# Kernel tuning notes

Hardware: AMD Instinct MI355X
Metric: run time of the kernel (lower is better)

The kernel has to match this reference:

```python
import jax, jax.numpy as jnp
import numpy as np

D = 768


def _rope(x):
    # interleaved RoPE over the FULL hidden dim (applied before head split, as in source)
    S, d = x.shape[-2], x.shape[-1]
    pos = jnp.arange(S, dtype=x.dtype)[:, None]                      # [S,1]
    theta = jnp.power(jnp.asarray(10000.0, x.dtype),
                      -2.0 * jnp.arange(d // 2, dtype=x.dtype) / d)  # [d/2]
    ang = pos * theta                                                # [S,d/2]
    cos2 = jnp.repeat(jnp.cos(ang), 2, axis=-1)                      # [S,d]
    sin2 = jnp.repeat(jnp.sin(ang), 2, axis=-1)
    x2 = jnp.stack([-x[..., 1::2], x[..., ::2]], axis=-1).reshape(x.shape)
    return x * cos2 + x2 * sin2


def _attn(q_in, kv_in, wq, bq, wk, bk, wv, bv, n_heads):
    # shared core of SelfAttention (n_heads=1) and MultiheadAttention (n_heads=8)
    B, Sq, Dm = q_in.shape
    Sk = kv_in.shape[1]
    Q = _rope(q_in @ wq + bq)
    K = _rope(kv_in @ wk + bk)
    V = kv_in @ wv + bv
    hd = Dm // n_heads
    Q = Q.reshape(B, Sq, n_heads, hd).transpose(0, 2, 1, 3)
    K = K.reshape(B, Sk, n_heads, hd).transpose(0, 2, 1, 3)
    V = V.reshape(B, Sk, n_heads, hd).transpose(0, 2, 1, 3)
    scores = jnp.einsum('bhqd,bhkd->bhqk', Q, K) * 8.0  # source multiplies by 8, no 1/sqrt(d)
    p = jax.nn.softmax(scores, axis=-1)
    out = jnp.einsum('bhqk,bhkd->bhqd', p, V)
    return out.transpose(0, 2, 1, 3).reshape(B, Sq, Dm)


def _ffn(x, w1, b1, w2, b2):
    return jax.nn.silu(x @ w1 + b1) @ w2 + b2


def _gate(x):
    # F = F * softmax(F, -1) + F
    return x * jax.nn.softmax(x, axis=-1) + x


def setup_inputs() -> dict:
    key = jax.random.key(0)
    ks = jax.random.split(key, 32)
    B, S, L = 32, 512, 100
    s = 1.0 / np.sqrt(D)

    def lin(k):
        kw, kb = jax.random.split(k)
        return (jax.random.normal(kw, (D, D), jnp.float32) * s,
                jax.random.normal(kb, (D,), jnp.float32) * 0.01)

    inp = {}
    inp['text_embedding'] = jax.random.normal(ks[0], (B, S, D), jnp.float32)
    inp['visual_ids'] = jax.random.randint(ks[1], (B, S), 0, L)
    inp['acoustic_ids'] = jax.random.randint(ks[2], (B, S), 0, L)
    # embedding tables (label_size+1 rows, last row is padding_idx -> zeros)
    vt = jax.random.normal(ks[3], (L + 1, D), jnp.float32)
    at = jax.random.normal(ks[4], (L + 1, D), jnp.float32)
    inp['vis_table'] = vt.at[L].set(0.0)
    inp['ac_table'] = at.at[L].set(0.0)
    (inp['hv_wq'], inp['hv_bq']) = lin(ks[5])
    (inp['hv_wk'], inp['hv_bk']) = lin(ks[6])
    (inp['hv_wv'], inp['hv_bv']) = lin(ks[7])
    (inp['ha_wq'], inp['ha_bq']) = lin(ks[8])
    (inp['ha_wk'], inp['ha_bk']) = lin(ks[9])
    (inp['ha_wv'], inp['ha_bv']) = lin(ks[10])
    (inp['ht_wq'], inp['ht_bq']) = lin(ks[11])
    (inp['ht_wk'], inp['ht_bk']) = lin(ks[12])
    (inp['ht_wv'], inp['ht_bv']) = lin(ks[13])
    (inp['ht_fcw'], inp['ht_fcb']) = lin(ks[14])
    (inp['ffn_w1'], inp['ffn_b1']) = lin(ks[15])
    (inp['ffn_w2'], inp['ffn_b2']) = lin(ks[16])
    kw, kb = jax.random.split(ks[17])
    inp['cat_w'] = jax.random.normal(kw, (2 * D, D), jnp.float32) * (1.0 / np.sqrt(2 * D))
    inp['cat_b'] = jax.random.normal(kb, (D,), jnp.float32) * 0.01
    return inp


def reference(text_embedding, vis_table, ac_table,
              hv_wq, hv_bq, hv_wk, hv_bk, hv_wv, hv_bv,
              ha_wq, ha_bq, ha_wk, ha_bk, ha_wv, ha_bv,
              ht_wq, ht_bq, ht_wk, ht_bk, ht_wv, ht_bv, ht_fcw, ht_fcb,
              ffn_w1, ffn_b1, ffn_w2, ffn_b2, cat_w, cat_b,
              visual_ids, acoustic_ids):
    hv = lambda q, kv: _attn(q, kv, hv_wq, hv_bq, hv_wk, hv_bk, hv_wv, hv_bv, 1)
    ha = lambda q, kv: _attn(q, kv, ha_wq, ha_bq, ha_wk, ha_bk, ha_wv, ha_bv, 1)

    visual_ = vis_table[visual_ids]       # [B,S,D]
    acoustic_ = ac_table[acoustic_ids]

    visual_ = hv(text_embedding, visual_)
    acoustic_ = ha(text_embedding, acoustic_)

    F1 = jnp.concatenate([visual_, acoustic_], axis=-1) @ cat_w + cat_b
    F1 = _ffn(_gate(F1), ffn_w1, ffn_b1, ffn_w2, ffn_b2)

    v = hv(visual_, acoustic_)
    a = ha(acoustic_, visual_)
    F2 = jnp.concatenate([v, a], axis=-1) @ cat_w + cat_b
    F2 = _ffn(_gate(F2), ffn_w1, ffn_b1, ffn_w2, ffn_b2)

    F3 = _attn(F1, text_embedding, ht_wq, ht_bq, ht_wk, ht_bk, ht_wv, ht_bv, 8)
    F3 = F3 @ ht_fcw + ht_fcb
    F3 = _ffn(_gate(F3), ffn_w1, ffn_b1, ffn_w2, ffn_b2)

    es = text_embedding + F1 + F2 + F3
    return _gate(es)
```

## Files before the change

### kernel.cpp

```cpp
#include <hip/hip_runtime.h>
#include <stdint.h>
#include <math.h>


typedef unsigned short USH;
typedef __attribute__((ext_vector_type(8))) short short8;
typedef __attribute__((ext_vector_type(4))) float floatx4;

#define MFMA16(a, b, c) __builtin_amdgcn_mfma_f32_16x16x32_bf16((a), (b), (c), 0, 0, 0)

static constexpr int NB = 32;
static constexpr int SS = 512;
static constexpr int DD = 768;
static constexpr int MM = NB * SS;

__device__ __forceinline__ float bf2f(USH h) {
    return __uint_as_float(((unsigned)h) << 16);
}
__device__ __forceinline__ USH f2bf(float x) {
    unsigned u = __float_as_uint(x);
    return (USH)((u + 0x7fffu + ((u >> 16) & 1u)) >> 16);
}
__device__ __forceinline__ void split3(float x, USH &h, USH &m, USH &l) {
    h = f2bf(x);
    const float r1 = x - bf2f(h);
    m = f2bf(r1);
    const float r2 = r1 - bf2f(m);
    l = f2bf(r2);
}
__device__ __forceinline__ void split3x8(const float* v, short8 &H, short8 &M, short8 &L) {
#pragma unroll
    for (int j = 0; j < 8; ++j) {
        USH h, m, l;
        split3(v[j], h, m, l);
        H[j] = (short)h; M[j] = (short)m; L[j] = (short)l;
    }
}
__device__ __forceinline__ uint2 pk4(USH a, USH b, USH c, USH d) {
    uint2 r;
    r.x = (unsigned)a | ((unsigned)b << 16);
    r.y = (unsigned)c | ((unsigned)d << 16);
    return r;
}

struct TransArgs {
    const float* in[13];
    USH* o0[13]; USH* o1[13]; USH* o2[13];
    int R[13];
};

__global__ __launch_bounds__(256) void trans_k(TransArgs a) {
    const int mi = blockIdx.z;
    const float* __restrict__ in = a.in[mi];
    USH* __restrict__ o0 = a.o0[mi];
    USH* __restrict__ o1 = a.o1[mi];
    USH* __restrict__ o2 = a.o2[mi];
    const int R = a.R[mi];
    const int bx = blockIdx.x, by = blockIdx.y;
    if (bx * 32 >= R) return;
    __shared__ float t[32][33];
    const int tx = threadIdx.x & 31, ty = threadIdx.x >> 5;
#pragma unroll
    for (int i = 0; i < 4; ++i)
        t[ty + i * 8][tx] = in[(size_t)(bx * 32 + ty + i * 8) * 768 + by * 32 + tx];
    __syncthreads();
#pragma unroll
    for (int i = 0; i < 4; ++i) {
        USH h, m, l;
        split3(t[tx][ty + i * 8], h, m, l);
        const size_t o = (size_t)(by * 32 + ty + i * 8) * R + bx * 32 + tx;
        o0[o] = h; o1[o] = m; o2[o] = l;
    }
}

__global__ __launch_bounds__(256) void gather_k(const int* __restrict__ ids,
                                                const float* __restrict__ table,
                                                float* __restrict__ dst) {
    const int g  = blockIdx.x * 256 + threadIdx.x;
    const int m  = g / 192;
    const int c4 = (g - m * 192) * 4;
    const int id = ids[m];
    *(float4*)(dst + (size_t)m * DD + c4) =
        *(const float4*)(table + (size_t)id * DD + c4);
}

__global__ __launch_bounds__(256) void gemm_k(
    const float* __restrict__ A0, const float* __restrict__ A1,
    const USH* __restrict__ B0, const USH* __restrict__ B1, const USH* __restrict__ B2,
    int ldb, const float* __restrict__ bias,
    float* __restrict__ C, USH* __restrict__ S0p, USH* __restrict__ S1p,
    USH* __restrict__ S2p, int K, int act, int tout, int Mc)
{
    __shared__ __align__(16) USH sA0[4096], sA1[4096], sA2[4096];
    __shared__ __align__(16) USH sB0[4096], sB1[4096], sB2[4096];

    const int tid  = threadIdx.x;
    const int lane = tid & 63;
    const int w    = tid >> 6;
    const int quad = lane >> 4, l15 = lane & 15;
    const int wm = (w >> 1) * 64, wn = (w & 1) * 64;
    const int gm0 = blockIdx.x * 128, gn0 = blockIdx.y * 128;

    const int i0 = tid * 2, i1 = tid * 2 + 1;
    const int r0 = i0 >> 2, c0 = (i0 & 3) << 3;
    const int r1 = i1 >> 2, c1 = (i1 & 3) << 3;

    const floatx4 zero = {0.f, 0.f, 0.f, 0.f};
    floatx4 acc[4][4];
#pragma unroll
    for (int i = 0; i < 4; ++i)
#pragma unroll
        for (int j = 0; j < 4; ++j) acc[i][j] = zero;

    for (int k0 = 0; k0 < K; k0 += 32) {
        const float* __restrict__ A = (k0 < 768) ? A0 : A1;
        const int kof = (k0 < 768) ? k0 : (k0 - 768);

        *(uint4*)&sB0[r0 * 32 + c0] = *(const uint4*)(B0 + (size_t)(gn0 + r0) * ldb + k0 + c0);
        *(uint4*)&sB0[r1 * 32 + c1] = *(const uint4*)(B0 + (size_t)(gn0 + r1) * ldb + k0 + c1);
        *(uint4*)&sB1[r0 * 32 + c0] = *(const uint4*)(B1 + (size_t)(gn0 + r0) * ldb + k0 + c0);
        *(uint4*)&sB1[r1 * 32 + c1] = *(const uint4*)(B1 + (size_t)(gn0 + r1) * ldb + k0 + c1);
        *(uint4*)&sB2[r0 * 32 + c0] = *(const uint4*)(B2 + (size_t)(gn0 + r0) * ldb + k0 + c0);
        *(uint4*)&sB2[r1 * 32 + c1] = *(const uint4*)(B2 + (size_t)(gn0 + r1) * ldb + k0 + c1);

#pragma unroll
        for (int u = 0; u < 4; ++u) {
            const int idx = tid + u * 256;
            const int r = idx >> 3, c = (idx & 7) * 4;
            const float4 v = *(const float4*)(A + (size_t)(gm0 + r) * 768 + kof + c);
            USH h[4], m[4], l[4];
            split3(v.x, h[0], m[0], l[0]);
            split3(v.y, h[1], m[1], l[1]);
            split3(v.z, h[2], m[2], l[2]);
            split3(v.w, h[3], m[3], l[3]);
            *(uint2*)&sA0[r * 32 + c] = pk4(h[0], h[1], h[2], h[3]);
            *(uint2*)&sA1[r * 32 + c] = pk4(m[0], m[1], m[2], m[3]);
            *(uint2*)&sA2[r * 32 + c] = pk4(l[0], l[1], l[2], l[3]);
        }
        __syncthreads();

        short8 a0[4], a1f[4], a2[4], b0[4], b1f[4], b2[4];
#pragma unroll
        for (int t = 0; t < 4; ++t) {
            const int ao = (wm + t * 16 + l15) * 32 + quad * 8;
            const int bo = (wn + t * 16 + l15) * 32 + quad * 8;
            a0[t]  = *(const short8*)&sA0[ao];
            a1f[t] = *(const short8*)&sA1[ao];
            a2[t]  = *(const short8*)&sA2[ao];
            b0[t]  = *(const short8*)&sB0[bo];
            b1f[t] = *(const short8*)&sB1[bo];
            b2[t]  = *(const short8*)&sB2[bo];
        }
#pragma unroll
        for (int i = 0; i < 4; ++i)
#pragma unroll
            for (int j = 0; j < 4; ++j) acc[i][j] = MFMA16(a0[i],  b0[j],  acc[i][j]);
#pragma unroll
        for (int i = 0; i < 4; ++i)
#pragma unroll
            for (int j = 0; j < 4; ++j) acc[i][j] = MFMA16(a0[i],  b1f[j], acc[i][j]);
#pragma unroll
        for (int i = 0; i < 4; ++i)
#pragma unroll
            for (int j = 0; j < 4; ++j) acc[i][j] = MFMA16(a1f[i], b0[j],  acc[i][j]);
#pragma unroll
        for (int i = 0; i < 4; ++i)
#pragma unroll
            for (int j = 0; j < 4; ++j) acc[i][j] = MFMA16(a0[i],  b2[j],  acc[i][j]);
#pragma unroll
        for (int i = 0; i < 4; ++i)
#pragma unroll
            for (int j = 0; j < 4; ++j) acc[i][j] = MFMA16(a2[i],  b0[j],  acc[i][j]);
#pragma unroll
        for (int i = 0; i < 4; ++i)
#pragma unroll
            for (int j = 0; j < 4; ++j) acc[i][j] = MFMA16(a1f[i], b1f[j], acc[i][j]);
        __syncthreads();
    }

#pragma unroll
    for (int j = 0; j < 4; ++j) {
        const int col = gn0 + wn + j * 16 + l15;
        const float bv = bias[col];
#pragma unroll
        for (int i = 0; i < 4; ++i) {
#pragma unroll
            for (int r = 0; r < 4; ++r) {
                const int row = gm0 + wm + i * 16 + quad * 4 + r;
                float x = acc[i][j][r] + bv;
                if (act == 1) {
                    const float s = 1.0f / (1.0f + expf(-x));
                    x = x * s;
                }
                if (tout == 1) {
                    USH hh, mm2, ll;
                    split3(x, hh, mm2, ll);
                    const size_t o = (size_t)col * Mc + row;
                    S0p[o] = hh; S1p[o] = mm2; S2p[o] = ll;
                } else if (tout == 2) {
                    C[(size_t)col * Mc + row] = x;
                } else {
                    C[(size_t)row * 768 + col] = x;
                }
            }
        }
    }
}

__global__ __launch_bounds__(256) void tab_k(float* __restrict__ tab) {
    const int p = blockIdx.x * 256 + threadIdx.x;
    const int s = p / 384;
    const int i = p - s * 384;
    const float ef = (-2.0f * (float)i) / 768.0f;
    const float th = (float)pow(10000.0, (double)ef);
    const float ang = (float)s * th;
    float sn, cs;
    sincosf(ang, &sn, &cs);
    tab[2 * p]     = cs;
    tab[2 * p + 1] = sn;
}

__global__ __launch_bounds__(256) void rope_k(float* __restrict__ X) {
    const int p = blockIdx.x * 256 + threadIdx.x;
    const int m = p / 384;
    const int i = p - m * 384;
    const int s = m & (SS - 1);
    const float ef = (-2.0f * (float)i) / 768.0f;
    const float th = (float)pow(10000.0, (double)ef);
    const float ang = (float)s * th;
    float sn, cs;
    sincosf(ang, &sn, &cs);
    float2 x = *(float2*)(X + (size_t)m * DD + 2 * i);
    float2 y;
    y.x = x.x * cs - x.y * sn;
    y.y = x.y * cs + x.x * sn;
    *(float2*)(X + (size_t)m * DD + 2 * i) = y;
}

__global__ __launch_bounds__(256) void rope_tab_k(float* __restrict__ X,
                                                  const float* __restrict__ tab) {
    const int p = blockIdx.x * 256 + threadIdx.x;
    const int m = p / 384;
    const int i = p - m * 384;
    const int s = m & (SS - 1);
    const float2 t = *(const float2*)(tab + 2 * (s * 384 + i));
    float2 x = *(float2*)(X + (size_t)m * DD + 2 * i);
    float2 y;
    y.x = x.x * t.x - x.y * t.y;
    y.y = x.y * t.x + x.x * t.y;
    *(float2*)(X + (size_t)m * DD + 2 * i) = y;
}

__global__ __launch_bounds__(256) void rope_split_tab_k(
    const float* __restrict__ X, const float* __restrict__ tab,
    USH* __restrict__ P0, USH* __restrict__ P1, USH* __restrict__ P2)
{
    const int p = blockIdx.x * 256 + threadIdx.x;
    const int m = p / 384;
    const int i = p - m * 384;
    const int s = m & (SS - 1);
    const float2 t = *(const float2*)(tab + 2 * (s * 384 + i));
    const float2 x = *(const float2*)(X + (size_t)m * DD + 2 * i);
    float2 y;
    y.x = x.x * t.x - x.y * t.y;
    y.y = x.y * t.x + x.x * t.y;
    USH h0, m0, l0, h1, m1, l1;
    split3(y.x, h0, m0, l0);
    split3(y.y, h1, m1, l1);
    const size_t o = (size_t)m * DD + 2 * i;
    *(unsigned*)&P0[o] = (unsigned)h0 | ((unsigned)h1 << 16);
    *(unsigned*)&P1[o] = (unsigned)m0 | ((unsigned)m1 << 16);
    *(unsigned*)&P2[o] = (unsigned)l0 | ((unsigned)l1 << 16);
}

__global__ __launch_bounds__(256) void attn_fast_k(
    const float* __restrict__ Q,
    const USH* __restrict__ KH, const USH* __restrict__ KM, const USH* __restrict__ KL,
    const USH* __restrict__ VH, const USH* __restrict__ VM, const USH* __restrict__ VL,
    float* __restrict__ O, int H, int hd, int Mc)
{
    __shared__ __align__(16) float S[16][520];
    __shared__ __align__(16) USH P2buf[16 * 520];
    __shared__ float red[16][16];
    __shared__ float stat[16];

    const int tid  = threadIdx.x;
    const int lane = tid & 63;
    const int w    = tid >> 6;
    const int quad = lane >> 4, l15 = lane & 15;
    const int b = blockIdx.y / H;
    const int h = blockIdx.y - b * H;
    const int q0 = blockIdx.x * 16;

    const floatx4 zero = {0.f, 0.f, 0.f, 0.f};

    floatx4 acc[8];
#pragma unroll
    for (int t = 0; t < 8; ++t) acc[t] = zero;

    const size_t qbase  = ((size_t)(b * SS + q0 + l15)) * DD + h * hd;
    const size_t kstrip = ((size_t)(b * SS + w * 128 + l15)) * DD + h * hd;
    const int nks = hd >> 5;
    for (int ks = 0; ks < nks; ++ks) {
        const int co = ks * 32 + quad * 8;
        float qv[8];
        *(float4*)&qv[0] = *(const float4*)(Q + qbase + co);
        *(float4*)&qv[4] = *(const float4*)(Q + qbase + co + 4);
        short8 qh, qm, ql;
        split3x8(qv, qh, qm, ql);

        size_t ka = kstrip + co;
        short8 khc = *(const short8*)&KH[ka];
        short8 kmc = *(const short8*)&KM[ka];
        short8 klc = *(const short8*)&KL[ka];
#pragma unroll
        for (int t = 0; t < 8; ++t) {
            short8 khn = khc, kmn = kmc, kln = klc;
            if (t < 7) {
                const size_t kb = ka + (size_t)(t + 1) * 16 * DD;
                khn = *(const short8*)&KH[kb];
                kmn = *(const short8*)&KM[kb];
                kln = *(const short8*)&KL[kb];
            }
            acc[t] = MFMA16(qh, khc, acc[t]);
            acc[t] = MFMA16(qh, kmc, acc[t]);
            acc[t] = MFMA16(qm, khc, acc[t]);
            acc[t] = MFMA16(qh, klc, acc[t]);
            acc[t] = MFMA16(ql, khc, acc[t]);
            acc[t] = MFMA16(qm, kmc, acc[t]);
            __builtin_amdgcn_sched_barrier(0);
            khc = khn; kmc = kmn; klc = kln;
        }
    }
#pragma unroll
    for (int t = 0; t < 8; ++t)
#pragma unroll
        for (int r = 0; r < 4; ++r)
            S[quad * 4 + r][w * 128 + t * 16 + l15] = acc[t][r] * 8.0f;
    __syncthreads();

    const int row = tid >> 4, c16 = tid & 15;
    const int cb = c16 * 32;
    float mx = -3.4e38f;
#pragma unroll 8
    for (int c = 0; c < 32; ++c) mx = fmaxf(mx, S[row][cb + c]);
    red[row][c16] = mx;
    __syncthreads();
    if (c16 == 0) {
        float m2 = red[row][0];
#pragma unroll
        for (int j = 1; j < 16; ++j) m2 = fmaxf(m2, red[row][j]);
        stat[row] = m2;
    }
    __syncthreads();
    mx = stat[row];
    float ev[32];
    float sum = 0.f;
#pragma unroll 8
    for (int c = 0; c < 32; ++c) {
        ev[c] = expf(S[row][cb + c] - mx);
        sum += ev[c];
    }
    red[row][c16] = sum;
    __syncthreads();
    if (c16 == 0) {
        float s2 = 0.f;
#pragma unroll
        for (int j = 0; j < 16; ++j) s2 += red[row][j];
        stat[row] = s2;
    }
    __syncthreads();
    const float den = stat[row];
    USH* const P0 = (USH*)&S[0][0];
    USH* const P1 = P0 + 16 * 520;
    USH* const P2 = P2buf;
#pragma unroll 8
    for (int c = 0; c < 32; ++c) {
        const float pr = ev[c] / den;
        USH hh, mm, ll;
        split3(pr, hh, mm, ll);
        P0[row * 520 + cb + c] = hh;
        P1[row * 520 + cb + c] = mm;
        P2[row * 520 + cb + c] = ll;
    }
    __syncthreads();

    const int nnt = hd >> 4;
    for (int nt = w; nt < nnt; nt += 4) {
        floatx4 o = zero;
        const int colg = h * hd + nt * 16 + l15;
        const size_t vb = (size_t)colg * Mc + b * SS;
#pragma unroll 2
        for (int ks = 0; ks < 16; ++ks) {
            const int ko = ks * 32 + quad * 8;
            const short8 ph = *(const short8*)&P0[l15 * 520 + ko];
            const short8 pm = *(const short8*)&P1[l15 * 520 + ko];
            const short8 pl = *(const short8*)&P2[l15 * 520 + ko];
            const short8 vh = *(const short8*)&VH[vb + ko];
            const short8 vm = *(const short8*)&VM[vb + ko];
            const short8 vl = *(const short8*)&VL[vb + ko];
            o = MFMA16(ph, vh, o);
            o = MFMA16(ph, vm, o);
            o = MFMA16(pm, vh, o);
            o = MFMA16(ph, vl, o);
            o = MFMA16(pl, vh, o);
            o = MFMA16(pm, vm, o);
        }
#pragma unroll
        for (int r = 0; r < 4; ++r) {
            const int orow = b * SS + q0 + quad * 4 + r;
            O[(size_t)orow * 768 + colg] = o[r];
        }
    }
}

__global__ __launch_bounds__(256) void attn_k(
    const float* __restrict__ Q, const float* __restrict__ Kp,
    const float* __restrict__ Vt, float* __restrict__ O,
    int H, int hd, int Mc)
{
    __shared__ __align__(16) float S[16][520];
    __shared__ __align__(16) USH P2buf[16 * 520];
    __shared__ float red[16][16];
    __shared__ float stat[16];

    const int tid  = threadIdx.x;
    const int lane = tid & 63;
    const int w    = tid >> 6;
    const int quad = lane >> 4, l15 = lane & 15;
    const int b = blockIdx.y / H;
    const int h = blockIdx.y - b * H;
    const int q0 = blockIdx.x * 16;

    const floatx4 zero = {0.f, 0.f, 0.f, 0.f};

    floatx4 acc[8];
#pragma unroll
    for (int t = 0; t < 8; ++t) acc[t] = zero;

    const size_t qbase = ((size_t)(b * SS + q0 + l15)) * DD + h * hd;
    const int nks = hd >> 5;
    for (int ks = 0; ks < nks; ++ks) {
        const int co = ks * 32 + quad * 8;
        float qv[8];
        *(float4*)&qv[0] = *(const float4*)(Q + qbase + co);
        *(float4*)&qv[4] = *(const float4*)(Q + qbase + co + 4);
        short8 qh, qm, ql;
        split3x8(qv, qh, qm, ql);
#pragma unroll
        for (int t = 0; t < 8; ++t) {
            const size_t kb = ((size_t)(b * SS + w * 128 + t * 16 + l15)) * DD + h * hd + co;
            float kv[8];
            *(float4*)&kv[0] = *(const float4*)(Kp + kb);
            *(float4*)&kv[4] = *(const float4*)(Kp + kb + 4);
            short8 kh, km, kl;
            split3x8(kv, kh, km, kl);
            acc[t] = MFMA16(qh, kh, acc[t]);
            acc[t] = MFMA16(qh, km, acc[t]);
            acc[t] = MFMA16(qm, kh, acc[t]);
            acc[t] = MFMA16(qh, kl, acc[t]);
            acc[t] = MFMA16(ql, kh, acc[t]);
            acc[t] = MFMA16(qm, km, acc[t]);
        }
    }
#pragma unroll
    for (int t = 0; t < 8; ++t)
#pragma unroll
        for (int r = 0; r < 4; ++r)
            S[quad * 4 + r][w * 128 + t * 16 + l15] = acc[t][r] * 8.0f;
    __syncthreads();

    const int row = tid >> 4, c16 = tid & 15;
    const int cb = c16 * 32;
    float mx = -3.4e38f;
#pragma unroll 8
    for (int c = 0; c < 32; ++c) mx = fmaxf(mx, S[row][cb + c]);
    red[row][c16] = mx;
    __syncthreads();
    if (c16 == 0) {
        float m2 = red[row][0];
#pragma unroll
        for (int j = 1; j < 16; ++j) m2 = fmaxf(m2, red[row][j]);
        stat[row] = m2;
    }
    __syncthreads();
    mx = stat[row];
    float ev[32];
    float sum = 0.f;
#pragma unroll 8
    for (int c = 0; c < 32; ++c) {
        ev[c] = expf(S[row][cb + c] - mx);
        sum += ev[c];
    }
    red[row][c16] = sum;
    __syncthreads();
    if (c16 == 0) {
        float s2 = 0.f;
#pragma unroll
        for (int j = 0; j < 16; ++j) s2 += red[row][j];
        stat[row] = s2;
    }
    __syncthreads();
    const float den = stat[row];
    USH* const P0 = (USH*)&S[0][0];
    USH* const P1 = P0 + 16 * 520;
    USH* const P2 = P2buf;
#pragma unroll 8
    for (int c = 0; c < 32; ++c) {
        const float pr = ev[c] / den;
        USH hh, mm, ll;
        split3(pr, hh, mm, ll);
        P0[row * 520 + cb + c] = hh;
        P1[row * 520 + cb + c] = mm;
        P2[row * 520 + cb + c] = ll;
    }
    __syncthreads();

    const int nnt = hd >> 4;
    for (int nt = w; nt < nnt; nt += 4) {
        floatx4 o = zero;
        const int colg = h * hd + nt * 16 + l15;
        const size_t vb = (size_t)colg * Mc + b * SS;
        for (int ks = 0; ks < 16; ++ks) {
            const int ko = ks * 32 + quad * 8;
            const short8 ph = *(const short8*)&P0[l15 * 520 + ko];
            const short8 pm = *(const short8*)&P1[l15 * 520 + ko];
            const short8 pl = *(const short8*)&P2[l15 * 520 + ko];
            float vv[8];
            *(float4*)&vv[0] = *(const float4*)(Vt + vb + ko);
            *(float4*)&vv[4] = *(const float4*)(Vt + vb + ko + 4);
            short8 vh, vm, vl;
            split3x8(vv, vh, vm, vl);
            o = MFMA16(ph, vh, o);
            o = MFMA16(ph, vm, o);
            o = MFMA16(pm, vh, o);
            o = MFMA16(ph, vl, o);
            o = MFMA16(pl, vh, o);
            o = MFMA16(pm, vm, o);
        }
#pragma unroll
        for (int r = 0; r < 4; ++r) {
            const int orow = b * SS + q0 + quad * 4 + r;
            O[(size_t)orow * 768 + colg] = o[r];
        }
    }
}

__global__ __launch_bounds__(256) void gate_k(float* __restrict__ X) {
    __shared__ float red[256];
    const int r = blockIdx.x, tid = threadIdx.x;
    const size_t base = (size_t)r * DD;
    float x[3];
#pragma unroll
    for (int j = 0; j < 3; ++j) x[j] = X[base + tid + j * 256];
    float mx = fmaxf(x[0], fmaxf(x[1], x[2]));
    red[tid] = mx;
    __syncthreads();
    for (int s = 128; s > 0; s >>= 1) {
        if (tid < s) red[tid] = fmaxf(red[tid], red[tid + s]);
        __syncthreads();
    }
    mx = red[0];
    __syncthreads();
    float e[3];
    float sum = 0.f;
#pragma unroll
    for (int j = 0; j < 3; ++j) { e[j] = expf(x[j] - mx); sum += e[j]; }
    red[tid] = sum;
    __syncthreads();
    for (int s = 128; s > 0; s >>= 1) {
        if (tid < s) red[tid] += red[tid + s];
        __syncthreads();
    }
    const float den = red[0];
#pragma unroll
    for (int j = 0; j < 3; ++j)
        X[base + tid + j * 256] = x[j] * (e[j] / den) + x[j];
}

__global__ __launch_bounds__(256) void final_k(
    const float* __restrict__ text,
    const float* __restrict__ F1, const float* __restrict__ F2,
    const float* __restrict__ F3, float* __restrict__ out)
{
    __shared__ float red[256];
    const int r = blockIdx.x, tid = threadIdx.x;
    const size_t base = (size_t)r * DD;
    float x[3];
#pragma unroll
    for (int j = 0; j < 3; ++j) {
        const int c = tid + j * 256;
        x[j] = ((text[base + c] + F1[base + c]) + F2[base + c]) + F3[base + c];
    }
    float mx = fmaxf(x[0], fmaxf(x[1], x[2]));
    red[tid] = mx;
    __syncthreads();
    for (int s = 128; s > 0; s >>= 1) {
        if (tid < s) red[tid] = fmaxf(red[tid], red[tid + s]);
        __syncthreads();
    }
    mx = red[0];
    __syncthreads();
    float e[3];
    float sum = 0.f;
#pragma unroll
    for (int j = 0; j < 3; ++j) { e[j] = expf(x[j] - mx); sum += e[j]; }
    red[tid] = sum;
    __syncthreads();
    for (int s = 128; s > 0; s >>= 1) {
        if (tid < s) red[tid] += red[tid + s];
        __syncthreads();
    }
    const float den = red[0];
#pragma unroll
    for (int j = 0; j < 3; ++j) {
        const int c = tid + j * 256;
        out[base + c] = x[j] * (e[j] / den) + x[j];
    }
}

extern "C" void kernel_launch(void* const* d_in, const int* in_sizes, int n_in,
                              void* d_out, int out_size, void* d_ws, size_t ws_size,
                              hipStream_t stream)
{
    (void)in_sizes; (void)n_in; (void)out_size;

    const float* text    = (const float*)d_in[0];
    const int*   vis_ids = (const int*)d_in[1];
    const int*   ac_ids  = (const int*)d_in[2];
    const float* vis_tab = (const float*)d_in[3];
    const float* ac_tab  = (const float*)d_in[4];
    const float* hv_wq = (const float*)d_in[5],  *hv_bq = (const float*)d_in[6];
    const float* hv_wk = (const float*)d_in[7],  *hv_bk = (const float*)d_in[8];
    const float* hv_wv = (const float*)d_in[9],  *hv_bv = (const float*)d_in[10];
    const float* ha_wq = (const float*)d_in[11], *ha_bq = (const float*)d_in[12];
    const float* ha_wk = (const float*)d_in[13], *ha_bk = (const float*)d_in[14];
    const float* ha_wv = (const float*)d_in[15], *ha_bv = (const float*)d_in[16];
    const float* ht_wq = (const float*)d_in[17], *ht_bq = (const float*)d_in[18];
    const float* ht_wk = (const float*)d_in[19], *ht_bk = (const float*)d_in[20];
    const float* ht_wv = (const float*)d_in[21], *ht_bv = (const float*)d_in[22];
    const float* ht_fcw = (const float*)d_in[23], *ht_fcb = (const float*)d_in[24];
    const float* ffn_w1 = (const float*)d_in[25], *ffn_b1 = (const float*)d_in[26];
    const float* ffn_w2 = (const float*)d_in[27], *ffn_b2 = (const float*)d_in[28];
    const float* cat_w  = (const float*)d_in[29], *cat_b  = (const float*)d_in[30];

    const size_t SQ   = (size_t)768 * 768;
    const size_t WUSH = 3 * (12 * SQ + (size_t)768 * 1536);
    const size_t TABF = (size_t)512 * 384 * 2;
    int Mc = 0, fast = 0;
    for (int cand = MM; cand >= 512; cand >>= 1) {
        const size_t nf = WUSH * sizeof(USH) + TABF * 4 + (size_t)cand * 768 * 28;
        const size_t ns = WUSH * sizeof(USH) + (size_t)cand * 768 * 24;
        if (nf <= ws_size) { Mc = cand; fast = 1; break; }
        if (ns <= ws_size) { Mc = cand; fast = 0; break; }
    }
    if (Mc == 0) return;
    const int nchunk = MM / Mc;
    const int chB    = Mc / SS;

    USH* p = (USH*)d_ws;
    USH *wt0[13], *wt1[13], *wt2[13];
    for (int i = 0; i < 13; ++i) {
        const size_t sz = (i == 12) ? (size_t)768 * 1536 : SQ;
        wt0[i] = p; p += sz;
        wt1[i] = p; p += sz;
        wt2[i] = p; p += sz;
    }

    TransArgs ta;
    const float* tin[13] = {hv_wq, hv_wk, hv_wv, ha_wq, ha_wk, ha_wv,
                            ht_wq, ht_wk, ht_wv, ht_fcw, ffn_w1, ffn_w2, cat_w};
    for (int i = 0; i < 13; ++i) {
        ta.in[i] = tin[i]; ta.o0[i] = wt0[i]; ta.o1[i] = wt1[i]; ta.o2[i] = wt2[i];
        ta.R[i] = (i == 12) ? 1536 : 768;
    }
    trans_k<<<dim3(48, 24, 13), 256, 0, stream>>>(ta);

    const size_t PSZ = (size_t)Mc * 768;
    const dim3 gg(Mc / 128, DD / 128), gb(256);
    const int ropeg = Mc * 384 / 256;
    const float* NULF = nullptr;
    USH* const NUSH = nullptr;

    if (fast) {
        float* tab = (float*)p;
        float* fp  = tab + TABF;
        float *A_ = fp + 0 * PSZ, *B_ = fp + 1 * PSZ;
        float *C_ = fp + 2 * PSZ, *F_ = fp + 3 * PSZ;
        USH* KH = (USH*)(fp + 4 * PSZ);
        USH* KM = KH + PSZ;  USH* KL = KM + PSZ;
        USH* VH = KL + PSZ;  USH* VM = VH + PSZ;  USH* VL = VM + PSZ;

        tab_k<<<(512 * 384) / 256, 256, 0, stream>>>(tab);

#define GEMM(A0P, A1P, WI, LDB, BIAS, CP, KK, ACT) \
    gemm_k<<<gg, gb, 0, stream>>>(A0P, A1P, wt0[WI], wt1[WI], wt2[WI], LDB, BIAS, \
                                  CP, NUSH, NUSH, NUSH, KK, ACT, 0, Mc)
#define GEMMV(A0P, WI, BIAS) \
    gemm_k<<<gg, gb, 0, stream>>>(A0P, NULF, wt0[WI], wt1[WI], wt2[WI], 768, BIAS, \
                                  (float*)nullptr, VH, VM, VL, 768, 0, 1, Mc)
#define ROPE(XP)  rope_tab_k<<<ropeg, 256, 0, stream>>>(XP, tab)
#define RSPL(XP)  rope_split_tab_k<<<ropeg, 256, 0, stream>>>(XP, tab, KH, KM, KL)
#define ATTNF(QP, OP, HH, HD) \
    attn_fast_k<<<dim3(SS / 16, chB * (HH)), 256, 0, stream>>>(QP, KH, KM, KL, \
                                                  VH, VM, VL, OP, HH, HD, Mc)
#define GATE(XP) gate_k<<<Mc, 256, 0, stream>>>(XP)

        for (int c = 0; c < nchunk; ++c) {
            const float* tx = text + (size_t)c * PSZ;
            const int* vi = vis_ids + (size_t)c * Mc;
            const int* ai = ac_ids  + (size_t)c * Mc;
            float* outc = (float*)d_out + (size_t)c * PSZ;

            gather_k<<<Mc * 192 / 256, 256, 0, stream>>>(vi, vis_tab, A_);
            gather_k<<<Mc * 192 / 256, 256, 0, stream>>>(ai, ac_tab, B_);

            GEMM(tx, NULF, 0, 768, hv_bq, C_, 768, 0);
            GEMM(A_, NULF, 1, 768, hv_bk, outc, 768, 0);
            GEMMV(A_, 2, hv_bv);
            ROPE(C_); RSPL(outc);
            ATTNF(C_, F_, 1, 768);

            GEMM(tx, NULF, 3, 768, ha_bq, C_, 768, 0);
            GEMM(B_, NULF, 4, 768, ha_bk, outc, 768, 0);
            GEMMV(B_, 5, ha_bv);
            ROPE(C_); RSPL(outc);
            ATTNF(C_, A_, 1, 768);

            GEMM(F_, NULF, 0, 768, hv_bq, C_, 768, 0);
            GEMM(A_, NULF, 1, 768, hv_bk, outc, 768, 0);
            GEMMV(A_, 2, hv_bv);
            ROPE(C_); RSPL(outc);
            ATTNF(C_, C_, 1, 768);

            GEMM(A_, NULF, 3, 768, ha_bq, B_, 768, 0);
            GEMM(F_, NULF, 4, 768, ha_bk, outc, 768, 0);
            GEMMV(F_, 5, ha_bv);
            ROPE(B_); RSPL(outc);
            ATTNF(B_, B_, 1, 768);

            GEMM(F_, A_, 12, 1536, cat_b, outc, 1536, 0);
            GATE(outc);
            GEMM(outc, NULF, 10, 768, ffn_b1, F_, 768, 1);
            GEMM(F_, NULF, 11, 768, ffn_b2, A_, 768, 0);

            GEMM(C_, B_, 12, 1536, cat_b, outc, 1536, 0);
            GATE(outc);
            GEMM(outc, NULF, 10, 768, ffn_b1, F_, 768, 1);
            GEMM(F_, NULF, 11, 768, ffn_b2, C_, 768, 0);

            GEMM(A_, NULF, 6, 768, ht_bq, B_, 768, 0);
            GEMM(tx, NULF, 7, 768, ht_bk, outc, 768, 0);
            GEMMV(tx, 8, ht_bv);
            ROPE(B_); RSPL(outc);
            ATTNF(B_, B_, 8, 96);
            GEMM(B_, NULF, 9, 768, ht_fcb, F_, 768, 0);
            GATE(F_);
            GEMM(F_, NULF, 10, 768, ffn_b1, B_, 768, 1);
            GEMM(B_, NULF, 11, 768, ffn_b2, F_, 768, 0);

            final_k<<<Mc, 256, 0, stream>>>(tx, A_, C_, F_, outc);
        }
#undef GEMM
#undef GEMMV
#undef ROPE
#undef RSPL
#undef ATTNF
#undef GATE
    } else {
        float* fp = (float*)p;
        float *A_ = fp + 0 * PSZ, *B_ = fp + 1 * PSZ, *C_ = fp + 2 * PSZ;
        float *D_ = fp + 3 * PSZ, *E_ = fp + 4 * PSZ, *F_ = fp + 5 * PSZ;

#define GEMM(A0P, A1P, WI, LDB, BIAS, CP, KK, ACT, TOUT) \
    gemm_k<<<gg, gb, 0, stream>>>(A0P, A1P, wt0[WI], wt1[WI], wt2[WI], LDB, BIAS, \
                                  CP, NUSH, NUSH, NUSH, KK, ACT, TOUT, Mc)
#define ROPE(XP) rope_k<<<ropeg, 256, 0, stream>>>(XP)
#define ATTN(QP, KP, VP, OP, HH, HD) \
    attn_k<<<dim3(SS / 16, chB * (HH)), 256, 0, stream>>>(QP, KP, VP, OP, HH, HD, Mc)
#define GATE(XP) gate_k<<<Mc, 256, 0, stream>>>(XP)

        for (int c = 0; c < nchunk; ++c) {
            const float* tx = text + (size_t)c * PSZ;
            const int* vi = vis_ids + (size_t)c * Mc;
            const int* ai = ac_ids  + (size_t)c * Mc;
            float* outc = (float*)d_out + (size_t)c * PSZ;

            gather_k<<<Mc * 192 / 256, 256, 0, stream>>>(vi, vis_tab, A_);
            gather_k<<<Mc * 192 / 256, 256, 0, stream>>>(ai, ac_tab, B_);

            GEMM(tx, NULF, 0, 768, hv_bq, C_, 768, 0, 0);
            GEMM(A_, NULF, 1, 768, hv_bk, D_, 768, 0, 0);
            GEMM(A_, NULF, 2, 768, hv_bv, E_, 768, 0, 2);
            ROPE(C_); ROPE(D_);
            ATTN(C_, D_, E_, F_, 1, 768);

            GEMM(tx, NULF, 3, 768, ha_bq, C_, 768, 0, 0);
            GEMM(B_, NULF, 4, 768, ha_bk, D_, 768, 0, 0);
            GEMM(B_, NULF, 5, 768, ha_bv, E_, 768, 0, 2);
            ROPE(C_); ROPE(D_);
            ATTN(C_, D_, E_, A_, 1, 768);

            GEMM(F_, NULF, 0, 768, hv_bq, C_, 768, 0, 0);
            GEMM(A_, NULF, 1, 768, hv_bk, D_, 768, 0, 0);
            GEMM(A_, NULF, 2, 768, hv_bv, E_, 768, 0, 2);
            ROPE(C_); ROPE(D_);
            ATTN(C_, D_, E_, C_, 1, 768);

            GEMM(A_, NULF, 3, 768, ha_bq, B_, 768, 0, 0);
            GEMM(F_, NULF, 4, 768, ha_bk, D_, 768, 0, 0);
            GEMM(F_, NULF, 5, 768, ha_bv, E_, 768, 0, 2);
            ROPE(B_); ROPE(D_);
            ATTN(B_, D_, E_, B_, 1, 768);

            GEMM(F_, A_, 12, 1536, cat_b, D_, 1536, 0, 0);
            GATE(D_);
            GEMM(D_, NULF, 10, 768, ffn_b1, E_, 768, 1, 0);
            GEMM(E_, NULF, 11, 768, ffn_b2, F_, 768, 0, 0);

            GEMM(C_, B_, 12, 1536, cat_b, A_, 1536, 0, 0);
            GATE(A_);
            GEMM(A_, NULF, 10, 768, ffn_b1, C_, 768, 1, 0);
            GEMM(C_, NULF, 11, 768, ffn_b2, B_, 768, 0, 0);

            GEMM(F_, NULF, 6, 768, ht_bq, C_, 768, 0, 0);
            GEMM(tx, NULF, 7, 768, ht_bk, D_, 768, 0, 0);
            GEMM(tx, NULF, 8, 768, ht_bv, E_, 768, 0, 2);
            ROPE(C_); ROPE(D_);
            ATTN(C_, D_, E_, C_, 8, 96);
            GEMM(C_, NULF, 9, 768, ht_fcb, A_, 768, 0, 0);
            GATE(A_);
            GEMM(A_, NULF, 10, 768, ffn_b1, C_, 768, 1, 0);
            GEMM(C_, NULF, 11, 768, ffn_b2, D_, 768, 0, 0);

            final_k<<<Mc, 256, 0, stream>>>(tx, F_, B_, D_, outc);
        }
#undef GEMM
#undef ROPE
#undef ATTN
#undef GATE
    }
}
```

Baseline: 7.340 ms.

## Fuse RoPE and split into GEMM epilogue, stage transposed stores, swizzle block order

Applies RoPE inside the GEMM epilogue, using a lane shuffle for the paired element and a precomputed table. This removes the separate rope_tab and rope_split kernels and their extra global round trips for Q and K. K is written directly as three bf16 split planes. The transposed V split output is staged through shared memory so global stores are coalesced, and both the GEMM and attention kernels remap block IDs across groups of eight, likely to improve cache locality. The risks are more epilogue work, such as the shuffle and table loads, and extra synchronisation in the transposed path.

```diff
diff --git a/kernel.cpp b/kernel.cpp
--- a/kernel.cpp
+++ b/kernel.cpp
@@ -82,129 +82,6 @@
     const int id = ids[m];
     *(float4*)(dst + (size_t)m * DD + c4) =
         *(const float4*)(table + (size_t)id * DD + c4);
-}
-
-__global__ __launch_bounds__(256) void gemm_k(
-    const float* __restrict__ A0, const float* __restrict__ A1,
-    const USH* __restrict__ B0, const USH* __restrict__ B1, const USH* __restrict__ B2,
-    int ldb, const float* __restrict__ bias,
-    float* __restrict__ C, USH* __restrict__ S0p, USH* __restrict__ S1p,
-    USH* __restrict__ S2p, int K, int act, int tout, int Mc)
-{
-    __shared__ __align__(16) USH sA0[4096], sA1[4096], sA2[4096];
-    __shared__ __align__(16) USH sB0[4096], sB1[4096], sB2[4096];
-
-    const int tid  = threadIdx.x;
-    const int lane = tid & 63;
-    const int w    = tid >> 6;
-    const int quad = lane >> 4, l15 = lane & 15;
-    const int wm = (w >> 1) * 64, wn = (w & 1) * 64;
-    const int gm0 = blockIdx.x * 128, gn0 = blockIdx.y * 128;
-
-    const int i0 = tid * 2, i1 = tid * 2 + 1;
-    const int r0 = i0 >> 2, c0 = (i0 & 3) << 3;
-    const int r1 = i1 >> 2, c1 = (i1 & 3) << 3;
-
-    const floatx4 zero = {0.f, 0.f, 0.f, 0.f};
-    floatx4 acc[4][4];
-#pragma unroll
-    for (int i = 0; i < 4; ++i)
-#pragma unroll
-        for (int j = 0; j < 4; ++j) acc[i][j] = zero;
-
-    for (int k0 = 0; k0 < K; k0 += 32) {
-        const float* __restrict__ A = (k0 < 768) ? A0 : A1;
-        const int kof = (k0 < 768) ? k0 : (k0 - 768);
-
-        *(uint4*)&sB0[r0 * 32 + c0] = *(const uint4*)(B0 + (size_t)(gn0 + r0) * ldb + k0 + c0);
-        *(uint4*)&sB0[r1 * 32 + c1] = *(const uint4*)(B0 + (size_t)(gn0 + r1) * ldb + k0 + c1);
-        *(uint4*)&sB1[r0 * 32 + c0] = *(const uint4*)(B1 + (size_t)(gn0 + r0) * ldb + k0 + c0);
-        *(uint4*)&sB1[r1 * 32 + c1] = *(const uint4*)(B1 + (size_t)(gn0 + r1) * ldb + k0 + c1);
-        *(uint4*)&sB2[r0 * 32 + c0] = *(const uint4*)(B2 + (size_t)(gn0 + r0) * ldb + k0 + c0);
-        *(uint4*)&sB2[r1 * 32 + c1] = *(const uint4*)(B2 + (size_t)(gn0 + r1) * ldb + k0 + c1);
-
-#pragma unroll
-        for (int u = 0; u < 4; ++u) {
-            const int idx = tid + u * 256;
-            const int r = idx >> 3, c = (idx & 7) * 4;
-            const float4 v = *(const float4*)(A + (size_t)(gm0 + r) * 768 + kof + c);
-            USH h[4], m[4], l[4];
-            split3(v.x, h[0], m[0], l[0]);
-            split3(v.y, h[1], m[1], l[1]);
-            split3(v.z, h[2], m[2], l[2]);
-            split3(v.w, h[3], m[3], l[3]);
-            *(uint2*)&sA0[r * 32 + c] = pk4(h[0], h[1], h[2], h[3]);
-            *(uint2*)&sA1[r * 32 + c] = pk4(m[0], m[1], m[2], m[3]);
-            *(uint2*)&sA2[r * 32 + c] = pk4(l[0], l[1], l[2], l[3]);
-        }
-        __syncthreads();
-
-        short8 a0[4], a1f[4], a2[4], b0[4], b1f[4], b2[4];
-#pragma unroll
-        for (int t = 0; t < 4; ++t) {
-            const int ao = (wm + t * 16 + l15) * 32 + quad * 8;
-            const int bo = (wn + t * 16 + l15) * 32 + quad * 8;
-            a0[t]  = *(const short8*)&sA0[ao];
-            a1f[t] = *(const short8*)&sA1[ao];
-            a2[t]  = *(const short8*)&sA2[ao];
-            b0[t]  = *(const short8*)&sB0[bo];
-            b1f[t] = *(const short8*)&sB1[bo];
-            b2[t]  = *(const short8*)&sB2[bo];
-        }
-#pragma unroll
-        for (int i = 0; i < 4; ++i)
-#pragma unroll
-            for (int j = 0; j < 4; ++j) acc[i][j] = MFMA16(a0[i],  b0[j],  acc[i][j]);
-#pragma unroll
-        for (int i = 0; i < 4; ++i)
-#pragma unroll
-            for (int j = 0; j < 4; ++j) acc[i][j] = MFMA16(a0[i],  b1f[j], acc[i][j]);
-#pragma unroll
-        for (int i = 0; i < 4; ++i)
-#pragma unroll
-            for (int j = 0; j < 4; ++j) acc[i][j] = MFMA16(a1f[i], b0[j],  acc[i][j]);
-#pragma unroll
-        for (int i = 0; i < 4; ++i)
-#pragma unroll
-            for (int j = 0; j < 4; ++j) acc[i][j] = MFMA16(a0[i],  b2[j],  acc[i][j]);
-#pragma unroll
-        for (int i = 0; i < 4; ++i)
-#pragma unroll
-            for (int j = 0; j < 4; ++j) acc[i][j] = MFMA16(a2[i],  b0[j],  acc[i][j]);
-#pragma unroll
-        for (int i = 0; i < 4; ++i)
-#pragma unroll
-            for (int j = 0; j < 4; ++j) acc[i][j] = MFMA16(a1f[i], b1f[j], acc[i][j]);
-        __syncthreads();
-    }
-
-#pragma unroll
-    for (int j = 0; j < 4; ++j) {
-        const int col = gn0 + wn + j * 16 + l15;
-        const float bv = bias[col];
-#pragma unroll
-        for (int i = 0; i < 4; ++i) {
-#pragma unroll
-            for (int r = 0; r < 4; ++r) {
-                const int row = gm0 + wm + i * 16 + quad * 4 + r;
-                float x = acc[i][j][r] + bv;
-                if (act == 1) {
-                    const float s = 1.0f / (1.0f + expf(-x));
-                    x = x * s;
-                }
-                if (tout == 1) {
-                    USH hh, mm2, ll;
-                    split3(x, hh, mm2, ll);
-                    const size_t o = (size_t)col * Mc + row;
-                    S0p[o] = hh; S1p[o] = mm2; S2p[o] = ll;
-                } else if (tout == 2) {
-                    C[(size_t)col * Mc + row] = x;
-                } else {
-                    C[(size_t)row * 768 + col] = x;
-                }
-            }
-        }
-    }
 }
 
 __global__ __launch_bounds__(256) void tab_k(float* __restrict__ tab) {
@@ -237,40 +114,180 @@
     *(float2*)(X + (size_t)m * DD + 2 * i) = y;
 }
 
-__global__ __launch_bounds__(256) void rope_tab_k(float* __restrict__ X,
-                                                  const float* __restrict__ tab) {
-    const int p = blockIdx.x * 256 + threadIdx.x;
-    const int m = p / 384;
-    const int i = p - m * 384;
-    const int s = m & (SS - 1);
-    const float2 t = *(const float2*)(tab + 2 * (s * 384 + i));
-    float2 x = *(float2*)(X + (size_t)m * DD + 2 * i);
-    float2 y;
-    y.x = x.x * t.x - x.y * t.y;
-    y.y = x.y * t.x + x.x * t.y;
-    *(float2*)(X + (size_t)m * DD + 2 * i) = y;
-}
-
-__global__ __launch_bounds__(256) void rope_split_tab_k(
-    const float* __restrict__ X, const float* __restrict__ tab,
-    USH* __restrict__ P0, USH* __restrict__ P1, USH* __restrict__ P2)
+__global__ __launch_bounds__(256) void gemm_k(
+    const float* __restrict__ A0, const float* __restrict__ A1,
+    const USH* __restrict__ B0, const USH* __restrict__ B1, const USH* __restrict__ B2,
+    int ldb, const float* __restrict__ bias,
+    float* __restrict__ C, USH* __restrict__ S0p, USH* __restrict__ S1p,
+    USH* __restrict__ S2p, const float* __restrict__ tab,
+    int K, int act, int tout, int rope, int Mc)
 {
-    const int p = blockIdx.x * 256 + threadIdx.x;
-    const int m = p / 384;
-    const int i = p - m * 384;
-    const int s = m & (SS - 1);
-    const float2 t = *(const float2*)(tab + 2 * (s * 384 + i));
-    const float2 x = *(const float2*)(X + (size_t)m * DD + 2 * i);
-    float2 y;
-    y.x = x.x * t.x - x.y * t.y;
-    y.y = x.y * t.x + x.x * t.y;
-    USH h0, m0, l0, h1, m1, l1;
-    split3(y.x, h0, m0, l0);
-    split3(y.y, h1, m1, l1);
-    const size_t o = (size_t)m * DD + 2 * i;
-    *(unsigned*)&P0[o] = (unsigned)h0 | ((unsigned)h1 << 16);
-    *(unsigned*)&P1[o] = (unsigned)m0 | ((unsigned)m1 << 16);
-    *(unsigned*)&P2[o] = (unsigned)l0 | ((unsigned)l1 << 16);
+    __shared__ __align__(16) USH smem[24576];
+    USH* const sA0 = smem;
+    USH* const sA1 = smem + 4096;
+    USH* const sA2 = smem + 8192;
+    USH* const sB0 = smem + 12288;
+    USH* const sB1 = smem + 16384;
+    USH* const sB2 = smem + 20480;
+
+    const int tid  = threadIdx.x;
+    const int lane = tid & 63;
+    const int w    = tid >> 6;
+    const int quad = lane >> 4, l15 = lane & 15;
+    const int wm = (w >> 1) * 64, wn = (w & 1) * 64;
+
+    const int nbx = gridDim.x;
+    const int tot = nbx * (int)gridDim.y;
+    int bid = blockIdx.y * nbx + blockIdx.x;
+    if ((tot & 7) == 0) bid = (bid & 7) * (tot >> 3) + (bid >> 3);
+    const int byy = bid / nbx;
+    const int gm0 = (bid - byy * nbx) * 128, gn0 = byy * 128;
+
+    const int i0 = tid * 2, i1 = tid * 2 + 1;
+    const int r0 = i0 >> 2, c0 = (i0 & 3) << 3;
+    const int r1 = i1 >> 2, c1 = (i1 & 3) << 3;
+
+    const floatx4 zero = {0.f, 0.f, 0.f, 0.f};
+    floatx4 acc[4][4];
+#pragma unroll
+    for (int i = 0; i < 4; ++i)
+#pragma unroll
+        for (int j = 0; j < 4; ++j) acc[i][j] = zero;
+
+    for (int k0 = 0; k0 < K; k0 += 32) {
+        const float* __restrict__ A = (k0 < 768) ? A0 : A1;
+        const int kof = (k0 < 768) ? k0 : (k0 - 768);
+
+        *(uint4*)&sB0[r0 * 32 + c0] = *(const uint4*)(B0 + (size_t)(gn0 + r0) * ldb + k0 + c0);
+        *(uint4*)&sB0[r1 * 32 + c1] = *(const uint4*)(B0 + (size_t)(gn0 + r1) * ldb + k0 + c1);
+        *(uint4*)&sB1[r0 * 32 + c0] = *(const uint4*)(B1 + (size_t)(gn0 + r0) * ldb + k0 + c0);
+        *(uint4*)&sB1[r1 * 32 + c1] = *(const uint4*)(B1 + (size_t)(gn0 + r1) * ldb + k0 + c1);
+        *(uint4*)&sB2[r0 * 32 + c0] = *(const uint4*)(B2 + (size_t)(gn0 + r0) * ldb + k0 + c0);
+        *(uint4*)&sB2[r1 * 32 + c1] = *(const uint4*)(B2 + (size_t)(gn0 + r1) * ldb + k0 + c1);
+
+#pragma unroll
+        for (int u = 0; u < 4; ++u) {
+            const int idx = tid + u * 256;
+            const int r = idx >> 3, c = (idx & 7) * 4;
+            const float4 v = *(const float4*)(A + (size_t)(gm0 + r) * 768 + kof + c);
+            USH h[4], m[4], l[4];
+            split3(v.x, h[0], m[0], l[0]);
+            split3(v.y, h[1], m[1], l[1]);
+            split3(v.z, h[2], m[2], l[2]);
+            split3(v.w, h[3], m[3], l[3]);
+            *(uint2*)&sA0[r * 32 + c] = pk4(h[0], h[1], h[2], h[3]);
+            *(uint2*)&sA1[r * 32 + c] = pk4(m[0], m[1], m[2], m[3]);
+            *(uint2*)&sA2[r * 32 + c] = pk4(l[0], l[1], l[2], l[3]);
+        }
+        __syncthreads();
+
+        short8 a0[4], a1f[4], a2[4], b0[4], b1f[4], b2[4];
+#pragma unroll
+        for (int t = 0; t < 4; ++t) {
+            const int ao = (wm + t * 16 + l15) * 32 + quad * 8;
+            const int bo = (wn + t * 16 + l15) * 32 + quad * 8;
+            a0[t]  = *(const short8*)&sA0[ao];
+            a1f[t] = *(const short8*)&sA1[ao];
+            a2[t]  = *(const short8*)&sA2[ao];
+            b0[t]  = *(const short8*)&sB0[bo];
+            b1f[t] = *(const short8*)&sB1[bo];
+            b2[t]  = *(const short8*)&sB2[bo];
+        }
+#pragma unroll
+        for (int i = 0; i < 4; ++i)
+#pragma unroll
+            for (int j = 0; j < 4; ++j) acc[i][j] = MFMA16(a0[i],  b0[j],  acc[i][j]);
+#pragma unroll
+        for (int i = 0; i < 4; ++i)
+#pragma unroll
+            for (int j = 0; j < 4; ++j) acc[i][j] = MFMA16(a0[i],  b1f[j], acc[i][j]);
+#pragma unroll
+        for (int i = 0; i < 4; ++i)
+#pragma unroll
+            for (int j = 0; j < 4; ++j) acc[i][j] = MFMA16(a1f[i], b0[j],  acc[i][j]);
+#pragma unroll
+        for (int i = 0; i < 4; ++i)
+#pragma unroll
+            for (int j = 0; j < 4; ++j) acc[i][j] = MFMA16(a0[i],  b2[j],  acc[i][j]);
+#pragma unroll
+        for (int i = 0; i < 4; ++i)
+#pragma unroll
+            for (int j = 0; j < 4; ++j) acc[i][j] = MFMA16(a2[i],  b0[j],  acc[i][j]);
+#pragma unroll
+        for (int i = 0; i < 4; ++i)
+#pragma unroll
+            for (int j = 0; j < 4; ++j) acc[i][j] = MFMA16(a1f[i], b1f[j], acc[i][j]);
+        __syncthreads();
+    }
+
+    if (tout == 1) {
+        USH* const sT = smem;
+#pragma unroll
+        for (int p = 0; p < 3; ++p) {
+            __syncthreads();
+#pragma unroll
+            for (int j = 0; j < 4; ++j) {
+                const int col = gn0 + wn + j * 16 + l15;
+                const int cl  = wn + j * 16 + l15;
+                const float bv = bias ? bias[col] : 0.0f;
+#pragma unroll
+                for (int i = 0; i < 4; ++i) {
+#pragma unroll
+                    for (int r = 0; r < 4; ++r) {
+                        const int rl = wm + i * 16 + quad * 4 + r;
+                        USH h, m, l;
+                        split3(acc[i][j][r] + bv, h, m, l);
+                        sT[cl * 144 + rl] = (p == 0) ? h : ((p == 1) ? m : l);
+                    }
+                }
+            }
+            __syncthreads();
+            USH* const dst = (p == 0) ? S0p : ((p == 1) ? S1p : S2p);
+#pragma unroll
+            for (int u = 0; u < 8; ++u) {
+                const int cc = u * 256 + tid;
+                const int cl = cc >> 4, off = (cc & 15) * 8;
+                *(short8*)(dst + (size_t)(gn0 + cl) * Mc + gm0 + off) =
+                    *(const short8*)&sT[cl * 144 + off];
+            }
+        }
+        return;
+    }
+
+#pragma unroll
+    for (int j = 0; j < 4; ++j) {
+        const int col = gn0 + wn + j * 16 + l15;
+        const float bv = bias ? bias[col] : 0.0f;
+#pragma unroll
+        for (int i = 0; i < 4; ++i) {
+#pragma unroll
+            for (int r = 0; r < 4; ++r) {
+                const int row = gm0 + wm + i * 16 + quad * 4 + r;
+                float x = acc[i][j][r] + bv;
+                if (act == 1) {
+                    const float s = 1.0f / (1.0f + expf(-x));
+                    x = x * s;
+                }
+                if (rope) {
+                    const float px = __shfl_xor(x, 1, 64);
+                    const float2 t = *(const float2*)(tab +
+                        2 * ((row & (SS - 1)) * 384 + (col >> 1)));
+                    x = (col & 1) ? (x * t.x + px * t.y)
+                                  : (x * t.x - px * t.y);
+                }
+                if (tout == 3) {
+                    USH h, m, l;
+                    split3(x, h, m, l);
+                    const size_t o = (size_t)row * 768 + col;
+                    S0p[o] = h; S1p[o] = m; S2p[o] = l;
+                } else if (tout == 2) {
+                    C[(size_t)col * Mc + row] = x;
+                } else {
+                    C[(size_t)row * 768 + col] = x;
+                }
+            }
+        }
+    }
 }
 
 __global__ __launch_bounds__(256) void attn_fast_k(
@@ -288,9 +305,15 @@
     const int lane = tid & 63;
     const int w    = tid >> 6;
     const int quad = lane >> 4, l15 = lane & 15;
-    const int b = blockIdx.y / H;
-    const int h = blockIdx.y - b * H;
-    const int q0 = blockIdx.x * 16;
+
+    const int nbx = gridDim.x;
+    const int tot = nbx * (int)gridDim.y;
+    int bid = blockIdx.y * nbx + blockIdx.x;
+    if ((tot & 7) == 0) bid = (bid & 7) * (tot >> 3) + (bid >> 3);
+    const int yy = bid / nbx;
+    const int q0 = (bid - yy * nbx) * 16;
+    const int b = yy / H;
+    const int h = yy - b * H;
 
     const floatx4 zero = {0.f, 0.f, 0.f, 0.f};
 
@@ -693,14 +716,18 @@
 
         tab_k<<<(512 * 384) / 256, 256, 0, stream>>>(tab);
 
-#define GEMM(A0P, A1P, WI, LDB, BIAS, CP, KK, ACT) \
+#define GE(A0P, A1P, WI, LDB, BIAS, CP, KK, ACT) \
     gemm_k<<<gg, gb, 0, stream>>>(A0P, A1P, wt0[WI], wt1[WI], wt2[WI], LDB, BIAS, \
-                                  CP, NUSH, NUSH, NUSH, KK, ACT, 0, Mc)
-#define GEMMV(A0P, WI, BIAS) \
+                                  CP, NUSH, NUSH, NUSH, tab, KK, ACT, 0, 0, Mc)
+#define GQ(A0P, WI, BIAS, CP) \
     gemm_k<<<gg, gb, 0, stream>>>(A0P, NULF, wt0[WI], wt1[WI], wt2[WI], 768, BIAS, \
-                                  (float*)nullptr, VH, VM, VL, 768, 0, 1, Mc)
-#define ROPE(XP)  rope_tab_k<<<ropeg, 256, 0, stream>>>(XP, tab)
-#define RSPL(XP)  rope_split_tab_k<<<ropeg, 256, 0, stream>>>(XP, tab, KH, KM, KL)
+                                  CP, NUSH, NUSH, NUSH, tab, 768, 0, 0, 1, Mc)
+#define GK(A0P, WI, BIAS) \
+    gemm_k<<<gg, gb, 0, stream>>>(A0P, NULF, wt0[WI], wt1[WI], wt2[WI], 768, BIAS, \
+                                  (float*)nullptr, KH, KM, KL, tab, 768, 0, 3, 1, Mc)
+#define GV(A0P, WI, BIAS) \
+    gemm_k<<<gg, gb, 0, stream>>>(A0P, NULF, wt0[WI], wt1[WI], wt2[WI], 768, BIAS, \
+                                  (float*)nullptr, VH, VM, VL, tab, 768, 0, 1, 0, Mc)
 #define ATTNF(QP, OP, HH, HD) \
     attn_fast_k<<<dim3(SS / 16, chB * (HH)), 256, 0, stream>>>(QP, KH, KM, KL, \
                                                   VH, VM, VL, OP, HH, HD, Mc)
@@ -715,56 +742,46 @@
             gather_k<<<Mc * 192 / 256, 256, 0, stream>>>(vi, vis_tab, A_);
             gather_k<<<Mc * 192 / 256, 256, 0, stream>>>(ai, ac_tab, B_);
 
-            GEMM(tx, NULF, 0, 768, hv_bq, C_, 768, 0);
-            GEMM(A_, NULF, 1, 768, hv_bk, outc, 768, 0);
-            GEMMV(A_, 2, hv_bv);
-            ROPE(C_); RSPL(outc);
+            GQ(tx, 0, hv_bq, C_);
+            GK(A_, 1, hv_bk);  GV(A_, 2, hv_bv);
             ATTNF(C_, F_, 1, 768);
 
-            GEMM(tx, NULF, 3, 768, ha_bq, C_, 768, 0);
-            GEMM(B_, NULF, 4, 768, ha_bk, outc, 768, 0);
-            GEMMV(B_, 5, ha_bv);
-            ROPE(C_); RSPL(outc);
+            GQ(tx, 3, ha_bq, C_);
+            GK(B_, 4, ha_bk);  GV(B_, 5, ha_bv);
             ATTNF(C_, A_, 1, 768);
 
-            GEMM(F_, NULF, 0, 768, hv_bq, C_, 768, 0);
-            GEMM(A_, NULF, 1, 768, hv_bk, outc, 768, 0);
-            GEMMV(A_, 2, hv_bv);
-            ROPE(C_); RSPL(outc);
+            GQ(F_, 0, hv_bq, C_);
+            GK(A_, 1, hv_bk);  GV(A_, 2, hv_bv);
             ATTNF(C_, C_, 1, 768);
 
-            GEMM(A_, NULF, 3, 768, ha_bq, B_, 768, 0);
-            GEMM(F_, NULF, 4, 768, ha_bk, outc, 768, 0);
-            GEMMV(F_, 5, ha_bv);
-            ROPE(B_); RSPL(outc);
+            GQ(A_, 3, ha_bq, B_);
+            GK(F_, 4, ha_bk);  GV(F_, 5, ha_bv);
             ATTNF(B_, B_, 1, 768);
 
-            GEMM(F_, A_, 12, 1536, cat_b, outc, 1536, 0);
+            GE(F_, A_, 12, 1536, cat_b, outc, 1536, 0);
             GATE(outc);
-            GEMM(outc, NULF, 10, 768, ffn_b1, F_, 768, 1);
-            GEMM(F_, NULF, 11, 768, ffn_b2, A_, 768, 0);
-
-            GEMM(C_, B_, 12, 1536, cat_b, outc, 1536, 0);
+            GE(outc, NULF, 10, 768, ffn_b1, F_, 768, 1);
+            GE(F_, NULF, 11, 768, ffn_b2, A_, 768, 0);
+
+            GE(C_, B_, 12, 1536, cat_b, outc, 1536, 0);
             GATE(outc);
-            GEMM(outc, NULF, 10, 768, ffn_b1, F_, 768, 1);
-            GEMM(F_, NULF, 11, 768, ffn_b2, C_, 768, 0);
-
-            GEMM(A_, NULF, 6, 768, ht_bq, B_, 768, 0);
-            GEMM(tx, NULF, 7, 768, ht_bk, outc, 768, 0);
-            GEMMV(tx, 8, ht_bv);
-            ROPE(B_); RSPL(outc);
+            GE(outc, NULF, 10, 768, ffn_b1, F_, 768, 1);
+            GE(F_, NULF, 11, 768, ffn_b2, C_, 768, 0);
+
+            GQ(A_, 6, ht_bq, B_);
+            GK(tx, 7, ht_bk);  GV(tx, 8, ht_bv);
             ATTNF(B_, B_, 8, 96);
-            GEMM(B_, NULF, 9, 768, ht_fcb, F_, 768, 0);
+            GE(B_, NULF, 9, 768, ht_fcb, F_, 768, 0);
             GATE(F_);
-            GEMM(F_, NULF, 10, 768, ffn_b1, B_, 768, 1);
-            GEMM(B_, NULF, 11, 768, ffn_b2, F_, 768, 0);
+            GE(F_, NULF, 10, 768, ffn_b1, B_, 768, 1);
+            GE(B_, NULF, 11, 768, ffn_b2, F_, 768, 0);
 
             final_k<<<Mc, 256, 0, stream>>>(tx, A_, C_, F_, outc);
         }
-#undef GEMM
-#undef GEMMV
-#undef ROPE
-#undef RSPL
+#undef GE
+#undef GQ
+#undef GK
+#undef GV
 #undef ATTNF
 #undef GATE
     } else {
@@ -774,7 +791,7 @@
 
 #define GEMM(A0P, A1P, WI, LDB, BIAS, CP, KK, ACT, TOUT) \
     gemm_k<<<gg, gb, 0, stream>>>(A0P, A1P, wt0[WI], wt1[WI], wt2[WI], LDB, BIAS, \
-                                  CP, NUSH, NUSH, NUSH, KK, ACT, TOUT, Mc)
+                                  CP, NUSH, NUSH, NUSH, NULF, KK, ACT, TOUT, 0, Mc)
 #define ROPE(XP) rope_k<<<ropeg, 256, 0, stream>>>(XP)
 #define ATTN(QP, KP, VP, OP, HH, HD) \
     attn_k<<<dim3(SS / 16, chB * (HH)), 256, 0, stream>>>(QP, KP, VP, OP, HH, HD, Mc)
```

Measured after the change: 7.309 ms. Within noise of the previous version (-0.4%).
